# Optimization experiments

Hardware: AMD Instinct MI355X
Metric: run time of the kernel (lower is better)

## Reference

```python
import jax, jax.numpy as jnp
import numpy as np

L, B, V, E, H = 128, 64, 10000, 512, 512


def setup_inputs() -> dict:
    key = jax.random.key(0)
    ks = jax.random.split(key, 12)
    s = 0.05
    seq = jax.random.randint(ks[0], (L, B), 0, V, dtype=jnp.int32)
    seq_length = jnp.full((B,), L, dtype=jnp.int32)  # equal lengths -> pack/pad identity
    return {
        "seq": seq,
        "seq_length": seq_length,
        "emb": jax.random.normal(ks[1], (V, E), jnp.float32) * 0.01,  # matches init.normal std=0.01
        "W_ih_f": jax.random.normal(ks[2], (3 * H, E), jnp.float32) * s,
        "W_hh_f": jax.random.normal(ks[3], (3 * H, H), jnp.float32) * s,
        "b_ih_f": jax.random.normal(ks[4], (3 * H,), jnp.float32) * s,
        "b_hh_f": jax.random.normal(ks[5], (3 * H,), jnp.float32) * s,
        "W_ih_b": jax.random.normal(ks[6], (3 * H, E), jnp.float32) * s,
        "W_hh_b": jax.random.normal(ks[7], (3 * H, H), jnp.float32) * s,
        "b_ih_b": jax.random.normal(ks[8], (3 * H,), jnp.float32) * s,
        "b_hh_b": jax.random.normal(ks[9], (3 * H,), jnp.float32) * s,
        "dec_W": jax.random.normal(ks[10], (V, 2 * H), jnp.float32) * s,
        "dec_b": jax.random.normal(ks[11], (V,), jnp.float32) * s,
    }


def _gru(x_emb, W_ih, W_hh, b_ih, b_hh, reverse):
    # x_emb: [L, B, E]; PyTorch GRU cell equations.
    gx = jnp.einsum('lbe,ge->lbg', x_emb, W_ih) + b_ih  # [L, B, 3H]
    h0 = jnp.zeros((x_emb.shape[1], W_hh.shape[1]), x_emb.dtype)

    def step(h, gx_t):
        gh = h @ W_hh.T + b_hh
        r = jax.nn.sigmoid(gx_t[:, :H] + gh[:, :H])
        z = jax.nn.sigmoid(gx_t[:, H:2 * H] + gh[:, H:2 * H])
        n = jnp.tanh(gx_t[:, 2 * H:] + r * gh[:, 2 * H:])
        h_new = (1.0 - z) * n + z * h
        return h_new, h_new

    _, ys = jax.lax.scan(step, h0, gx, reverse=reverse)
    return ys  # [L, B, H], aligned with input positions


def reference(seq, seq_length, emb, W_ih_f, W_hh_f, b_ih_f, b_hh_f,
              W_ih_b, W_hh_b, b_ih_b, b_hh_b, dec_W, dec_b):
    x = emb[seq]  # [L, B, E]; dropout=0 (eval) -> identity
    out_f = _gru(x, W_ih_f, W_hh_f, b_ih_f, b_hh_f, reverse=False)  # [L, B, H]
    out_b = _gru(x, W_ih_b, W_hh_b, b_ih_b, b_hh_b, reverse=True)   # [L, B, H]
    # EditType.REPLACE: fwd state before the edited token, bwd state after it
    out = jnp.concatenate([out_f[0:L - 2], out_b[2:L]], axis=2)  # [L-2, B, 2H]
    logits = jnp.einsum('lbh,vh->lbv', out, dec_W) + dec_b       # [L-2, B, V]
    return jax.nn.log_softmax(logits, axis=-1)
```

## Files before the change

kernel.cpp:

```cpp
#include <hip/hip_runtime.h>
#include <hip/hip_bf16.h>
#include <stdint.h>

#define LL 128
#define BB 64
#define VV 10000
#define EE 512
#define HH 512
#define G3 1536
#define MROWS 8192
#define DM 8064
#define D2H 1024
#define NPAD 10112
#define FP 16

typedef __bf16 bf16x8 __attribute__((ext_vector_type(8)));
typedef float f32x4 __attribute__((ext_vector_type(4)));
typedef int i32x4 __attribute__((ext_vector_type(4)));
typedef unsigned int u32x4 __attribute__((ext_vector_type(4)));
typedef unsigned short u16;
typedef unsigned long long u64;

static __device__ __forceinline__ float bf2f(u16 u) {
  unsigned int x = ((unsigned int)u) << 16;
  return __builtin_bit_cast(float, x);
}
static __device__ __forceinline__ u16 f2bf(float f) {
  unsigned int x = __builtin_bit_cast(unsigned int, f);
  unsigned int r = x + 0x7FFFu + ((x >> 16) & 1u);
  return (u16)(r >> 16);
}
static __device__ __forceinline__ signed char q8(float v) {
  float r = fminf(fmaxf(rintf(v), -127.f), 127.f);
  return (signed char)(int)r;
}

static __device__ __forceinline__ void cstore16(void* p, u32x4 v) {
  asm volatile("global_store_dwordx4 %0, %1, off sc0 sc1" :: "v"(p), "v"(v) : "memory");
}
static __device__ __forceinline__ void flagstore4(void* p, int v) {
  asm volatile("global_store_dword %0, %1, off sc0 sc1" :: "v"(p), "v"(v) : "memory");
}
static __device__ __forceinline__ int flagload4(const void* p) {
  int v;
  asm volatile("global_load_dword %0, %1, off sc0 sc1\n\ts_waitcnt vmcnt(0)"
               : "=v"(v) : "v"(p) : "memory");
  return v;
}
static __device__ __forceinline__ void gload_lds16(const void* g, void* s) {
  __builtin_amdgcn_global_load_lds(
      (const __attribute__((address_space(1))) unsigned int*)g,
      (__attribute__((address_space(3))) unsigned int*)s, 16, 0, 0);
}

__global__ void k_cast(const float4* __restrict__ src, ushort4* __restrict__ dst, int n4) {
  int i = blockIdx.x * blockDim.x + threadIdx.x;
  if (i < n4) {
    float4 v = src[i];
    ushort4 o;
    o.x = f2bf(v.x); o.y = f2bf(v.y); o.z = f2bf(v.z); o.w = f2bf(v.w);
    dst[i] = o;
  }
}

__global__ __launch_bounds__(256) void k_quant_w(const float* __restrict__ W,
                                                 signed char* __restrict__ Q,
                                                 float* __restrict__ wscale) {
  const int v = blockIdx.x;
  const int tid = threadIdx.x;
  const int l = tid & 63, w = tid >> 6;
  float4 x = *(const float4*)(W + (long)v * 1024 + tid * 4);
  float m = fmaxf(fmaxf(fabsf(x.x), fabsf(x.y)), fmaxf(fabsf(x.z), fabsf(x.w)));
#pragma unroll
  for (int off = 32; off; off >>= 1) m = fmaxf(m, __shfl_xor(m, off));
  __shared__ float red[4];
  __shared__ float s_inv;
  if (l == 0) red[w] = m;
  __syncthreads();
  if (tid == 0) {
    float mm = fmaxf(fmaxf(red[0], red[1]), fmaxf(red[2], red[3]));
    mm = fmaxf(mm, 1e-12f);
    s_inv = 127.f / mm;
    wscale[v] = mm / (127.f * 127.f);
  }
  __syncthreads();
  float inv = s_inv;
  char4 o;
  o.x = q8(x.x * inv); o.y = q8(x.y * inv); o.z = q8(x.z * inv); o.w = q8(x.w * inv);
  *(char4*)(Q + (long)v * 1024 + tid * 4) = o;
}

__global__ void k_embed(const int* __restrict__ seq, const float* __restrict__ emb,
                        u16* __restrict__ x) {
  int rb = blockIdx.x;
  int v = seq[rb];
  const float4* s = (const float4*)(emb + (long)v * EE);
  ushort4* d = (ushort4*)(x + (long)rb * EE);
  int t = threadIdx.x;
  float4 val = s[t];
  ushort4 o;
  o.x = f2bf(val.x); o.y = f2bf(val.y); o.z = f2bf(val.z); o.w = f2bf(val.w);
  d[t] = o;
}

template<int OUTF32>
__global__ __launch_bounds__(256) void k_gemm(
    const u16* __restrict__ A, const u16* __restrict__ B,
    const float* __restrict__ bias, void* __restrict__ C,
    int lda, int ldb, int ldc, int K, int ncols)
{
  __shared__ char smem[32768];
  const int tid = threadIdx.x;
  const int l = tid & 63;
  const int w = tid >> 6;
  const int wr = w >> 1, wc = w & 1;
  const long tM = (long)blockIdx.x * 128;
  const long tN = (long)blockIdx.y * 128;

  f32x4 acc[4][4];
#pragma unroll
  for (int m = 0; m < 4; m++)
#pragma unroll
    for (int n = 0; n < 4; n++) acc[m][n] = {0.f, 0.f, 0.f, 0.f};

  const int nk = K >> 6;
  for (int kt = 0; kt < nk; ++kt) {
    const int k0 = kt << 6;
#pragma unroll
    for (int i = 0; i < 4; i++) {
      int cchunk = w * 4 + i;
      int c = cchunk * 64 + l;
      int row = c >> 3, k8 = c & 7;
      gload_lds16(A + (tM + row) * lda + k0 + k8 * 8, smem + cchunk * 1024);
      gload_lds16(B + (tN + row) * ldb + k0 + k8 * 8, smem + 16384 + cchunk * 1024);
    }
    __syncthreads();
#pragma unroll
    for (int kk = 0; kk < 2; kk++) {
      const int kb = kk * 64 + ((l >> 4) * 16);
      bf16x8 af[4], bfr[4];
#pragma unroll
      for (int m = 0; m < 4; m++) {
        int ra = wr * 64 + m * 16 + (l & 15);
        af[m] = *(const bf16x8*)(smem + ra * 128 + kb);
      }
#pragma unroll
      for (int n = 0; n < 4; n++) {
        int rb2 = wc * 64 + n * 16 + (l & 15);
        bfr[n] = *(const bf16x8*)(smem + 16384 + rb2 * 128 + kb);
      }
#pragma unroll
      for (int m = 0; m < 4; m++)
#pragma unroll
        for (int n = 0; n < 4; n++)
          acc[m][n] = __builtin_amdgcn_mfma_f32_16x16x32_bf16(af[m], bfr[n], acc[m][n], 0, 0, 0);
    }
    __syncthreads();
  }
#pragma unroll
  for (int n = 0; n < 4; n++) {
    long col = tN + wc * 64 + n * 16 + (l & 15);
    float bv = (col < ncols) ? bias[col] : 0.f;
    if (col < ncols) {
#pragma unroll
      for (int m = 0; m < 4; m++) {
        long row = tM + wr * 64 + m * 16 + ((l >> 4) * 4);
#pragma unroll
        for (int r = 0; r < 4; r++) {
          float v = acc[m][n][r] + bv;
          if (OUTF32) ((float*)C)[(row + r) * ldc + col] = v;
          else        ((u16*)C)[(row + r) * ldc + col] = f2bf(v);
        }
      }
    }
  }
}

__global__ __launch_bounds__(256) void k_gemm_i8(
    const signed char* __restrict__ A,
    const signed char* __restrict__ B,
    const float* __restrict__ wscale,
    const float* __restrict__ bias,
    float* __restrict__ C)
{
  __shared__ char smem[32768];
  const int tid = threadIdx.x;
  const int l = tid & 63;
  const int w = tid >> 6;
  const int wr = w >> 1, wc = w & 1;
  const long tM = (long)blockIdx.x * 128;
  const long tN = (long)blockIdx.y * 128;

  i32x4 acc[4][4];
#pragma unroll
  for (int m = 0; m < 4; m++)
#pragma unroll
    for (int n = 0; n < 4; n++) acc[m][n] = {0, 0, 0, 0};

  for (int kt = 0; kt < 8; ++kt) {
    const int k0 = kt << 7;
#pragma unroll
    for (int i = 0; i < 4; i++) {
      int j = w * 4 + i;
      int row = j * 8 + (l >> 3);
      int k16 = l & 7;
      gload_lds16(A + (tM + row) * 1024 + k0 + k16 * 16, smem + j * 1024);
      gload_lds16(B + (tN + row) * 1024 + k0 + k16 * 16, smem + 16384 + j * 1024);
    }
    __syncthreads();
#pragma unroll
    for (int ks = 0; ks < 2; ks++) {
      const int kb = ks * 64 + ((l >> 4) * 16);
      i32x4 af[4], bfr[4];
#pragma unroll
      for (int m = 0; m < 4; m++) {
        int ra = wr * 64 + m * 16 + (l & 15);
        af[m] = *(const i32x4*)(smem + ra * 128 + kb);
      }
#pragma unroll
      for (int n = 0; n < 4; n++) {
        int rb2 = wc * 64 + n * 16 + (l & 15);
        bfr[n] = *(const i32x4*)(smem + 16384 + rb2 * 128 + kb);
      }
#pragma unroll
      for (int m = 0; m < 4; m++)
#pragma unroll
        for (int n = 0; n < 4; n++)
          acc[m][n] = __builtin_amdgcn_mfma_i32_16x16x64_i8(af[m], bfr[n], acc[m][n], 0, 0, 0);
    }
    __syncthreads();
  }
#pragma unroll
  for (int n = 0; n < 4; n++) {
    long col = tN + wc * 64 + n * 16 + (l & 15);
    if (col < VV) {
      float sc = wscale[col];
      float bv = bias[col];
#pragma unroll
      for (int m = 0; m < 4; m++) {
        long row = tM + wr * 64 + m * 16 + ((l >> 4) * 4);
#pragma unroll
        for (int r = 0; r < 4; r++)
          C[(row + r) * VV + col] = (float)acc[m][n][r] * sc + bv;
      }
    }
  }
}

__global__ __launch_bounds__(256) void k_gru(
    const u16* __restrict__ Whh_all,
    const float* __restrict__ bhh_f, const float* __restrict__ bhh_b,
    const u16* __restrict__ gx_all,
    u16* __restrict__ hsteps,
    signed char* __restrict__ catq,
    int* __restrict__ bar16)
{
  const int blk = blockIdx.x;
  const int dir = blockIdx.y;
  const int tid = threadIdx.x;
  const int l = tid & 63, w = tid >> 6;
  const u16* Whh = Whh_all + (long)dir * G3 * HH;
  const float* bhh = dir ? bhh_b : bhh_f;
  const u16* gx = gx_all + (long)dir * MROWS * G3;

  __shared__ char Wl[96 * 1024];
  __shared__ __align__(16) u16 hstage[BB][32];
  __shared__ __align__(8) signed char hstageq[BB][32];

  for (int c = tid; c < 6144; c += 256) {
    int lr = c >> 6;
    int k8 = c & 63;
    int gr = (lr >> 5) * HH + blk * 32 + (lr & 31);
    uint4 v = *(const uint4*)(Whh + (long)gr * HH + k8 * 8);
    *(uint4*)(Wl + lr * 1024 + ((k8 * 16) ^ ((lr & 7) << 4))) = v;
  }
  float bh[6];
#pragma unroll
  for (int n = 0; n < 6; n++) {
    int c = n * 16 + (l & 15);
    bh[n] = bhh[(c >> 5) * HH + blk * 32 + (c & 31)];
  }
  float hreg[4][2] = {};
  __syncthreads();

  const int lrow = w * 16 + ((l >> 4) * 4);
  const int srow = tid >> 2, schunk = tid & 3;

  u16 gxn[3][4][2];
  {
    const int lpos0 = dir ? (LL - 1) : 0;
#pragma unroll
    for (int r = 0; r < 4; r++) {
      const u16* gxr = gx + ((long)lpos0 * BB + (lrow + r)) * G3 + blk * 32;
#pragma unroll
      for (int g = 0; g < 3; g++)
#pragma unroll
        for (int p = 0; p < 2; p++)
          gxn[g][r][p] = gxr[g * HH + p * 16 + (l & 15)];
    }
  }

  for (int t = 0; t < LL; ++t) {
    const int lpos = dir ? (LL - 1 - t) : t;
    const u16* hsrc = hsteps + ((size_t)t * 2 + dir) * BB * HH;

    u16 gxv[3][4][2];
#pragma unroll
    for (int g = 0; g < 3; g++)
#pragma unroll
      for (int r = 0; r < 4; r++)
#pragma unroll
        for (int p = 0; p < 2; p++) gxv[g][r][p] = gxn[g][r][p];

    bf16x8 af[16];
    {
      const u16* hrow = hsrc + (w * 16 + (l & 15)) * HH + ((l >> 4) * 8);
#pragma unroll
      for (int kc = 0; kc < 16; kc++) af[kc] = *(const bf16x8*)(hrow + kc * 32);
    }

    f32x4 acc[6];
#pragma unroll
    for (int n = 0; n < 6; n++) acc[n] = {0.f, 0.f, 0.f, 0.f};
#pragma unroll
    for (int kc = 0; kc < 16; kc++) {
      const int kb = kc * 64 + ((l >> 4) * 16);
#pragma unroll
      for (int n = 0; n < 6; n++) {
        int lr = n * 16 + (l & 15);
        bf16x8 bfr = *(const bf16x8*)(Wl + lr * 1024 + (kb ^ ((l & 7) << 4)));
        acc[n] = __builtin_amdgcn_mfma_f32_16x16x32_bf16(af[kc], bfr, acc[n], 0, 0, 0);
      }
    }

#pragma unroll
    for (int r = 0; r < 4; r++) {
#pragma unroll
      for (int p = 0; p < 2; p++) {
        float ghr = acc[0 + p][r] + bh[0 + p];
        float ghz = acc[2 + p][r] + bh[2 + p];
        float ghn = acc[4 + p][r] + bh[4 + p];
        float xr = bf2f(gxv[0][r][p]);
        float xz = bf2f(gxv[1][r][p]);
        float xn = bf2f(gxv[2][r][p]);
        float ar = fminf(fmaxf(xr + ghr, -30.f), 30.f);
        float az = fminf(fmaxf(xz + ghz, -30.f), 30.f);
        float rg = 1.f / (1.f + __expf(-ar));
        float zg = 1.f / (1.f + __expf(-az));
        float an = fminf(fmaxf(xn + rg * ghn, -30.f), 30.f);
        float e2 = __expf(-2.f * an);
        float ng = (1.f - e2) / (1.f + e2);
        float hn = (1.f - zg) * ng + zg * hreg[r][p];
        hreg[r][p] = hn;
        hstage[lrow + r][p * 16 + (l & 15)] = f2bf(hn);
        hstageq[lrow + r][p * 16 + (l & 15)] = q8(hn * 127.f);
      }
    }
    __syncthreads();

    u32x4 hv = *(const u32x4*)&hstage[srow][schunk * 8];
    u64 hq = *(const u64*)&hstageq[srow][schunk * 8];
    if (t < LL - 1) {
      u16* hdst = hsteps + ((size_t)(t + 1) * 2 + dir) * BB * HH;
      cstore16(hdst + srow * HH + blk * 32 + schunk * 8, hv);
      asm volatile("s_waitcnt vmcnt(0)" ::: "memory");
      __syncthreads();
      if (tid == 0)
        flagstore4(&bar16[((dir * LL + t) * 16 + blk) * FP], 1);
      {
        const int lposn = dir ? (LL - 2 - t) : (t + 1);
#pragma unroll
        for (int r = 0; r < 4; r++) {
          const u16* gxr = gx + ((long)lposn * BB + (lrow + r)) * G3 + blk * 32;
#pragma unroll
          for (int g = 0; g < 3; g++)
#pragma unroll
            for (int p = 0; p < 2; p++)
              gxn[g][r][p] = gxr[g * HH + p * 16 + (l & 15)];
        }
      }
      if (dir == 0) {
        if (lpos < LL - 2)
          *(u64*)(catq + ((long)lpos * BB + srow) * D2H + blk * 32 + schunk * 8) = hq;
      } else {
        if (lpos >= 2)
          *(u64*)(catq + ((long)(lpos - 2) * BB + srow) * D2H + HH + blk * 32 + schunk * 8) = hq;
      }
      const int* flg = bar16 + (dir * LL + t) * 16 * FP;
      for (;;) {
        int v = 1;
        if (l < 16) v = flagload4(&flg[l * FP]);
        if (__all(v != 0)) break;
      }
      __builtin_amdgcn_sched_barrier(0);
    } else {
      if (dir == 0) {
        if (lpos < LL - 2)
          *(u64*)(catq + ((long)lpos * BB + srow) * D2H + blk * 32 + schunk * 8) = hq;
      } else {
        if (lpos >= 2)
          *(u64*)(catq + ((long)(lpos - 2) * BB + srow) * D2H + HH + blk * 32 + schunk * 8) = hq;
      }
    }
  }
}

__global__ __launch_bounds__(256) void k_lsm(float* __restrict__ out) {
  const long row = blockIdx.x;
  float* p = out + row * VV;
  const int tid = threadIdx.x;
  const int l = tid & 63, w = tid >> 6;
  __shared__ float red[8];

  float4 v[10];
  float m = -1e30f;
#pragma unroll
  for (int j = 0; j < 10; j++) {
    int idx = j * 256 + tid;
    if (idx < 2500) {
      v[j] = *(float4*)(p + idx * 4);
      m = fmaxf(m, fmaxf(fmaxf(v[j].x, v[j].y), fmaxf(v[j].z, v[j].w)));
    }
  }
#pragma unroll
  for (int off = 32; off; off >>= 1) m = fmaxf(m, __shfl_xor(m, off));
  if (l == 0) red[w] = m;
  __syncthreads();
  m = fmaxf(fmaxf(red[0], red[1]), fmaxf(red[2], red[3]));

  float s = 0.f;
#pragma unroll
  for (int j = 0; j < 10; j++) {
    int idx = j * 256 + tid;
    if (idx < 2500) {
      s += __expf(v[j].x - m) + __expf(v[j].y - m) + __expf(v[j].z - m) + __expf(v[j].w - m);
    }
  }
#pragma unroll
  for (int off = 32; off; off >>= 1) s += __shfl_xor(s, off);
  if (l == 0) red[4 + w] = s;
  __syncthreads();
  s = red[4] + red[5] + red[6] + red[7];
  float lse = m + logf(s);

#pragma unroll
  for (int j = 0; j < 10; j++) {
    int idx = j * 256 + tid;
    if (idx < 2500) {
      float4 o;
      o.x = v[j].x - lse; o.y = v[j].y - lse; o.z = v[j].z - lse; o.w = v[j].w - lse;
      *(float4*)(p + idx * 4) = o;
    }
  }
}

extern "C" void kernel_launch(void* const* d_in, const int* in_sizes, int n_in,
                              void* d_out, int out_size, void* d_ws, size_t ws_size,
                              hipStream_t stream) {
  const int*   seq  = (const int*)d_in[0];
  const float* emb  = (const float*)d_in[2];
  const float* Wihf = (const float*)d_in[3];
  const float* Whhf = (const float*)d_in[4];
  const float* bihf = (const float*)d_in[5];
  const float* bhhf = (const float*)d_in[6];
  const float* Wihb = (const float*)d_in[7];
  const float* Whhb = (const float*)d_in[8];
  const float* bihb = (const float*)d_in[9];
  const float* bhhb = (const float*)d_in[10];
  const float* decW = (const float*)d_in[11];
  const float* decb = (const float*)d_in[12];

  char* ws = (char*)d_ws;
  size_t off = 0;
  u16* Whh_bf = (u16*)(ws + off); off += (size_t)2 * G3 * HH * 2;
  u16* Wih_bf = (u16*)(ws + off); off += (size_t)2 * G3 * EE * 2;
  signed char* decWq = (signed char*)(ws + off); off += (size_t)NPAD * 1024;
  float* wscale = (float*)(ws + off); off += (size_t)NPAD * 4;
  u16* xb = (u16*)(ws + off); off += (size_t)MROWS * EE * 2;
  u16* gxb = (u16*)(ws + off); off += (size_t)2 * MROWS * G3 * 2;
  signed char* catq = (signed char*)(ws + off); off += (size_t)DM * D2H;
  u16* hsteps = (u16*)(ws + off); off += (size_t)(LL + 1) * 2 * BB * HH * 2;
  int* bar16 = (int*)(ws + off); off += (size_t)2 * LL * 16 * FP * 4;

  (void)hipMemsetAsync(hsteps, 0, (size_t)2 * BB * HH * 2, stream);
  (void)hipMemsetAsync(bar16, 0, (size_t)2 * LL * 16 * FP * 4, stream);

  const int n4w = G3 * HH / 4;
  k_cast<<<(n4w + 255) / 256, 256, 0, stream>>>((const float4*)Whhf, (ushort4*)(Whh_bf), n4w);
  k_cast<<<(n4w + 255) / 256, 256, 0, stream>>>((const float4*)Whhb, (ushort4*)(Whh_bf + G3 * HH), n4w);
  k_cast<<<(n4w + 255) / 256, 256, 0, stream>>>((const float4*)Wihf, (ushort4*)(Wih_bf), n4w);
  k_cast<<<(n4w + 255) / 256, 256, 0, stream>>>((const float4*)Wihb, (ushort4*)(Wih_bf + G3 * EE), n4w);
  k_quant_w<<<VV, 256, 0, stream>>>(decW, decWq, wscale);
  k_embed<<<MROWS, 128, 0, stream>>>(seq, emb, xb);

  k_gemm<0><<<dim3(64, 12), 256, 0, stream>>>(xb, Wih_bf, bihf, gxb, EE, EE, G3, EE, G3);
  k_gemm<0><<<dim3(64, 12), 256, 0, stream>>>(xb, Wih_bf + G3 * EE, bihb, gxb + (size_t)MROWS * G3, EE, EE, G3, EE, G3);

  k_gru<<<dim3(16, 2), 256, 0, stream>>>(Whh_bf, bhhf, bhhb, gxb, hsteps, catq, bar16);

  k_gemm_i8<<<dim3(63, 79), 256, 0, stream>>>(catq, decWq, wscale, decb, (float*)d_out);

  k_lsm<<<DM, 256, 0, stream>>>((float*)d_out);
}
```

Baseline: 1.183 ms.

## Stage decoder logits in bf16 workspace and merge cast and gx GEMM launches

The int8 decoder GEMM now writes bf16 logits to a padded workspace buffer when the workspace is large enough. A new log-softmax kernel reads those bf16 values and writes the final fp32 output, replacing the fp32 write-then-read-modify-write of the full logits tensor. The four weight-cast launches are folded into one 2D-grid launch, and the two input-projection GEMMs run as one launch using blockIdx.z. This trims logits traffic and launch overhead, at the cost of rounding the logits to bf16 before log-softmax and relying on workspace size.

```diff
diff --git a/kernel.cpp b/kernel.cpp
--- a/kernel.cpp
+++ b/kernel.cpp
@@ -53,13 +53,23 @@
       (__attribute__((address_space(3))) unsigned int*)s, 16, 0, 0);
 }
 
-__global__ void k_cast(const float4* __restrict__ src, ushort4* __restrict__ dst, int n4) {
+__global__ void k_cast4(const float4* __restrict__ s0, const float4* __restrict__ s1,
+                        const float4* __restrict__ s2, const float4* __restrict__ s3,
+                        ushort4* __restrict__ d0, ushort4* __restrict__ d1,
+                        ushort4* __restrict__ d2, ushort4* __restrict__ d3, int n4) {
+  const float4* s; ushort4* d;
+  switch (blockIdx.y) {
+    case 0: s = s0; d = d0; break;
+    case 1: s = s1; d = d1; break;
+    case 2: s = s2; d = d2; break;
+    default: s = s3; d = d3; break;
+  }
   int i = blockIdx.x * blockDim.x + threadIdx.x;
   if (i < n4) {
-    float4 v = src[i];
+    float4 v = s[i];
     ushort4 o;
     o.x = f2bf(v.x); o.y = f2bf(v.y); o.z = f2bf(v.z); o.w = f2bf(v.w);
-    dst[i] = o;
+    d[i] = o;
   }
 }
 
@@ -103,11 +113,9 @@
   d[t] = o;
 }
 
-template<int OUTF32>
-__global__ __launch_bounds__(256) void k_gemm(
-    const u16* __restrict__ A, const u16* __restrict__ B,
-    const float* __restrict__ bias, void* __restrict__ C,
-    int lda, int ldb, int ldc, int K, int ncols)
+__global__ __launch_bounds__(256) void k_gemm_gx(
+    const u16* __restrict__ A, const u16* __restrict__ W0, const u16* __restrict__ W1,
+    const float* __restrict__ b0, const float* __restrict__ b1, u16* __restrict__ C)
 {
   __shared__ char smem[32768];
   const int tid = threadIdx.x;
@@ -116,6 +124,10 @@
   const int wr = w >> 1, wc = w & 1;
   const long tM = (long)blockIdx.x * 128;
   const long tN = (long)blockIdx.y * 128;
+  const int z = blockIdx.z;
+  const u16* B = z ? W1 : W0;
+  const float* bias = z ? b1 : b0;
+  u16* Cz = C + (size_t)z * MROWS * G3;
 
   f32x4 acc[4][4];
 #pragma unroll
@@ -123,16 +135,15 @@
 #pragma unroll
     for (int n = 0; n < 4; n++) acc[m][n] = {0.f, 0.f, 0.f, 0.f};
 
-  const int nk = K >> 6;
-  for (int kt = 0; kt < nk; ++kt) {
+  for (int kt = 0; kt < 8; ++kt) {
     const int k0 = kt << 6;
 #pragma unroll
     for (int i = 0; i < 4; i++) {
       int cchunk = w * 4 + i;
       int c = cchunk * 64 + l;
       int row = c >> 3, k8 = c & 7;
-      gload_lds16(A + (tM + row) * lda + k0 + k8 * 8, smem + cchunk * 1024);
-      gload_lds16(B + (tN + row) * ldb + k0 + k8 * 8, smem + 16384 + cchunk * 1024);
+      gload_lds16(A + (tM + row) * EE + k0 + k8 * 8, smem + cchunk * 1024);
+      gload_lds16(B + (tN + row) * EE + k0 + k8 * 8, smem + 16384 + cchunk * 1024);
     }
     __syncthreads();
 #pragma unroll
@@ -160,28 +171,24 @@
 #pragma unroll
   for (int n = 0; n < 4; n++) {
     long col = tN + wc * 64 + n * 16 + (l & 15);
-    float bv = (col < ncols) ? bias[col] : 0.f;
-    if (col < ncols) {
-#pragma unroll
-      for (int m = 0; m < 4; m++) {
-        long row = tM + wr * 64 + m * 16 + ((l >> 4) * 4);
-#pragma unroll
-        for (int r = 0; r < 4; r++) {
-          float v = acc[m][n][r] + bv;
-          if (OUTF32) ((float*)C)[(row + r) * ldc + col] = v;
-          else        ((u16*)C)[(row + r) * ldc + col] = f2bf(v);
-        }
-      }
-    }
-  }
-}
-
+    float bv = bias[col];
+#pragma unroll
+    for (int m = 0; m < 4; m++) {
+      long row = tM + wr * 64 + m * 16 + ((l >> 4) * 4);
+#pragma unroll
+      for (int r = 0; r < 4; r++)
+        Cz[(row + r) * G3 + col] = f2bf(acc[m][n][r] + bv);
+    }
+  }
+}
+
+template<int OUTBF16>
 __global__ __launch_bounds__(256) void k_gemm_i8(
     const signed char* __restrict__ A,
     const signed char* __restrict__ B,
     const float* __restrict__ wscale,
     const float* __restrict__ bias,
-    float* __restrict__ C)
+    void* __restrict__ Cv)
 {
   __shared__ char smem[32768];
   const int tid = threadIdx.x;
@@ -240,8 +247,11 @@
       for (int m = 0; m < 4; m++) {
         long row = tM + wr * 64 + m * 16 + ((l >> 4) * 4);
 #pragma unroll
-        for (int r = 0; r < 4; r++)
-          C[(row + r) * VV + col] = (float)acc[m][n][r] * sc + bv;
+        for (int r = 0; r < 4; r++) {
+          float vv = (float)acc[m][n][r] * sc + bv;
+          if (OUTBF16) ((u16*)Cv)[(row + r) * NPAD + col] = f2bf(vv);
+          else         ((float*)Cv)[(row + r) * VV + col] = vv;
+        }
       }
     }
   }
@@ -454,6 +464,66 @@
   }
 }
 
+__global__ __launch_bounds__(256) void k_lsm_b(const u16* __restrict__ lg,
+                                               float* __restrict__ out) {
+  const long row = blockIdx.x;
+  const u16* p = lg + row * NPAD;
+  float* q = out + row * VV;
+  const int tid = threadIdx.x;
+  const int l = tid & 63, w = tid >> 6;
+  __shared__ float red[8];
+
+  float v[5][8];
+  float m = -1e30f;
+#pragma unroll
+  for (int j = 0; j < 5; j++) {
+    int idx8 = j * 256 + tid;
+    if (idx8 < 1250) {
+      u32x4 u = *(const u32x4*)(p + idx8 * 8);
+#pragma unroll
+      for (int e = 0; e < 4; e++) {
+        v[j][2 * e]     = bf2f((u16)(u[e] & 0xffffu));
+        v[j][2 * e + 1] = bf2f((u16)(u[e] >> 16));
+      }
+#pragma unroll
+      for (int e = 0; e < 8; e++) m = fmaxf(m, v[j][e]);
+    }
+  }
+#pragma unroll
+  for (int off = 32; off; off >>= 1) m = fmaxf(m, __shfl_xor(m, off));
+  if (l == 0) red[w] = m;
+  __syncthreads();
+  m = fmaxf(fmaxf(red[0], red[1]), fmaxf(red[2], red[3]));
+
+  float s = 0.f;
+#pragma unroll
+  for (int j = 0; j < 5; j++) {
+    int idx8 = j * 256 + tid;
+    if (idx8 < 1250) {
+#pragma unroll
+      for (int e = 0; e < 8; e++) s += __expf(v[j][e] - m);
+    }
+  }
+#pragma unroll
+  for (int off = 32; off; off >>= 1) s += __shfl_xor(s, off);
+  if (l == 0) red[4 + w] = s;
+  __syncthreads();
+  s = red[4] + red[5] + red[6] + red[7];
+  float lse = m + logf(s);
+
+#pragma unroll
+  for (int j = 0; j < 5; j++) {
+    int idx8 = j * 256 + tid;
+    if (idx8 < 1250) {
+      float4 a, b;
+      a.x = v[j][0] - lse; a.y = v[j][1] - lse; a.z = v[j][2] - lse; a.w = v[j][3] - lse;
+      b.x = v[j][4] - lse; b.y = v[j][5] - lse; b.z = v[j][6] - lse; b.w = v[j][7] - lse;
+      *(float4*)(q + idx8 * 8) = a;
+      *(float4*)(q + idx8 * 8 + 4) = b;
+    }
+  }
+}
+
 extern "C" void kernel_launch(void* const* d_in, const int* in_sizes, int n_in,
                               void* d_out, int out_size, void* d_ws, size_t ws_size,
                               hipStream_t stream) {
@@ -481,24 +551,31 @@
   signed char* catq = (signed char*)(ws + off); off += (size_t)DM * D2H;
   u16* hsteps = (u16*)(ws + off); off += (size_t)(LL + 1) * 2 * BB * HH * 2;
   int* bar16 = (int*)(ws + off); off += (size_t)2 * LL * 16 * FP * 4;
+  u16* logitsb = (u16*)(ws + off);
+  const size_t logits_bytes = (size_t)DM * NPAD * 2;
+  const bool use_bf16_logits = (ws_size >= off + logits_bytes);
 
   (void)hipMemsetAsync(hsteps, 0, (size_t)2 * BB * HH * 2, stream);
   (void)hipMemsetAsync(bar16, 0, (size_t)2 * LL * 16 * FP * 4, stream);
 
   const int n4w = G3 * HH / 4;
-  k_cast<<<(n4w + 255) / 256, 256, 0, stream>>>((const float4*)Whhf, (ushort4*)(Whh_bf), n4w);
-  k_cast<<<(n4w + 255) / 256, 256, 0, stream>>>((const float4*)Whhb, (ushort4*)(Whh_bf + G3 * HH), n4w);
-  k_cast<<<(n4w + 255) / 256, 256, 0, stream>>>((const float4*)Wihf, (ushort4*)(Wih_bf), n4w);
-  k_cast<<<(n4w + 255) / 256, 256, 0, stream>>>((const float4*)Wihb, (ushort4*)(Wih_bf + G3 * EE), n4w);
+  k_cast4<<<dim3((n4w + 255) / 256, 4), 256, 0, stream>>>(
+      (const float4*)Whhf, (const float4*)Whhb, (const float4*)Wihf, (const float4*)Wihb,
+      (ushort4*)Whh_bf, (ushort4*)(Whh_bf + G3 * HH),
+      (ushort4*)Wih_bf, (ushort4*)(Wih_bf + G3 * EE), n4w);
   k_quant_w<<<VV, 256, 0, stream>>>(decW, decWq, wscale);
   k_embed<<<MROWS, 128, 0, stream>>>(seq, emb, xb);
 
-  k_gemm<0><<<dim3(64, 12), 256, 0, stream>>>(xb, Wih_bf, bihf, gxb, EE, EE, G3, EE, G3);
-  k_gemm<0><<<dim3(64, 12), 256, 0, stream>>>(xb, Wih_bf + G3 * EE, bihb, gxb + (size_t)MROWS * G3, EE, EE, G3, EE, G3);
+  k_gemm_gx<<<dim3(64, 12, 2), 256, 0, stream>>>(xb, Wih_bf, Wih_bf + G3 * EE,
+                                                 bihf, bihb, gxb);
 
   k_gru<<<dim3(16, 2), 256, 0, stream>>>(Whh_bf, bhhf, bhhb, gxb, hsteps, catq, bar16);
 
-  k_gemm_i8<<<dim3(63, 79), 256, 0, stream>>>(catq, decWq, wscale, decb, (float*)d_out);
-
-  k_lsm<<<DM, 256, 0, stream>>>((float*)d_out);
-}
+  if (use_bf16_logits) {
+    k_gemm_i8<1><<<dim3(63, 79), 256, 0, stream>>>(catq, decWq, wscale, decb, logitsb);
+    k_lsm_b<<<DM, 256, 0, stream>>>(logitsb, (float*)d_out);
+  } else {
+    k_gemm_i8<0><<<dim3(63, 79), 256, 0, stream>>>(catq, decWq, wscale, decb, d_out);
+    k_lsm<<<DM, 256, 0, stream>>>((float*)d_out);
+  }
+}
```

Result: faster. 1.098 ms (-7.2%).
